# Kernel optimization log

Hardware: AMD Instinct MI355X
Metric: run time of the kernel (lower is better)

The kernel has to match this reference:

```python
import jax, jax.numpy as jnp
import numpy as np

B, S, H = 1, 2048, 4096
NQ, NKV, HD = 32, 8, 128
BLOCK = 128            # block size of block_streaming_attn_func
SINK_BLOCKS = 1        # sink_size 128 / BLOCK
LOCAL_BLOCKS = 8       # local_window_size 1024 / BLOCK
ROPE_BASE = 10000.0


def setup_inputs() -> dict:
    key = jax.random.key(0)
    ks = jax.random.split(key, 5)
    s = 0.02
    return {
        "hidden_states": jax.random.normal(ks[0], (B, S, H), jnp.float32),
        "wq": jax.random.normal(ks[1], (H, NQ * HD), jnp.float32) * s,
        "wk": jax.random.normal(ks[2], (H, NKV * HD), jnp.float32) * s,
        "wv": jax.random.normal(ks[3], (H, NKV * HD), jnp.float32) * s,
        "wo": jax.random.normal(ks[4], (NQ * HD, H), jnp.float32) * s,
    }


def _rope(x):
    # x: [B, S, heads, HD]; non-interleaved (GPT-NeoX half-split) rotary, full head_dim
    pos = jnp.arange(S, dtype=jnp.float32)
    inv = 1.0 / (ROPE_BASE ** (jnp.arange(0, HD, 2, dtype=jnp.float32) / HD))
    f = pos[:, None] * inv[None, :]                 # [S, HD/2]
    cos = jnp.cos(f)[None, :, None, :]
    sin = jnp.sin(f)[None, :, None, :]
    x1, x2 = x[..., : HD // 2], x[..., HD // 2 :]
    return jnp.concatenate([x1 * cos - x2 * sin, x2 * cos + x1 * sin], axis=-1).astype(x.dtype)


def _streaming_mask():
    # causal + (sink blocks OR local window blocks), block granularity = BLOCK
    idx = jnp.arange(S)
    blk = idx // BLOCK
    causal = idx[None, :] <= idx[:, None]
    sink = blk[None, :] < SINK_BLOCKS
    local = (blk[:, None] - blk[None, :]) < LOCAL_BLOCKS
    return causal & (sink | local)                  # [S, S]


def reference(hidden_states, wq, wk, wv, wo):
    q = (hidden_states @ wq).reshape(B, S, NQ, HD)
    k = (hidden_states @ wk).reshape(B, S, NKV, HD)
    v = (hidden_states @ wv).reshape(B, S, NKV, HD)
    q = _rope(q)
    k = _rope(k)
    rep = NQ // NKV                                 # repeat_kv (GQA)
    k = jnp.repeat(k, rep, axis=2)
    v = jnp.repeat(v, rep, axis=2)
    scores = jnp.einsum('bqhd,bkhd->bhqk', q, k) / jnp.sqrt(jnp.float32(HD))
    mask = _streaming_mask()
    scores = jnp.where(mask[None, None], scores, jnp.finfo(scores.dtype).min)
    p = jax.nn.softmax(scores, axis=-1)
    out = jnp.einsum('bhqk,bkhd->bqhd', p, v).reshape(B, S, NQ * HD)
    return out @ wo
```

## Files before the change

kernel.cpp:

```cpp
#include <hip/hip_runtime.h>
#include <hip/hip_bf16.h>
#include <math.h>

typedef __bf16 bf16;
typedef __attribute__((ext_vector_type(8))) __bf16 bf16x8;
typedef __attribute__((ext_vector_type(4))) __bf16 bf16x4;
typedef __attribute__((ext_vector_type(4))) float f32x4;

#define MFMA16(a, b, c) __builtin_amdgcn_mfma_f32_16x16x32_bf16(a, b, c, 0, 0, 0)

__device__ __forceinline__ void load16_lds(const bf16* g, bf16* l) {
  __builtin_amdgcn_global_load_lds(
      (const __attribute__((address_space(1))) void*)g,
      (__attribute__((address_space(3))) void*)l, 16, 0, 0);
}

__global__ __launch_bounds__(256) void cast_k(const float* __restrict__ src,
                                              bf16* __restrict__ dst) {
  const size_t i = ((size_t)blockIdx.x * 256 + threadIdx.x) * 8;
  f32x4 a = *(const f32x4*)(src + i);
  f32x4 b = *(const f32x4*)(src + i + 4);
  bf16x8 h;
#pragma unroll
  for (int j = 0; j < 4; ++j) {
    h[j] = (bf16)a[j];
    h[4 + j] = (bf16)b[j];
  }
  *(bf16x8*)(dst + i) = h;
}

__global__ __launch_bounds__(256) void transpose_cast_k(
    const float* __restrict__ src, bf16* __restrict__ dst, int rows,
    int cols) {
  __shared__ float tile[64][65];
  const int c0 = blockIdx.x * 64, r0 = blockIdx.y * 64;
  const int tid = threadIdx.x;
  const int lr = tid >> 4;
  const int lc = (tid & 15) * 4;
#pragma unroll
  for (int i = 0; i < 4; ++i) {
    const int row = lr + i * 16;
    const f32x4 v = *(const f32x4*)&src[(size_t)(r0 + row) * cols + c0 + lc];
#pragma unroll
    for (int j = 0; j < 4; ++j) tile[row][lc + j] = v[j];
  }
  __syncthreads();
#pragma unroll
  for (int i = 0; i < 4; ++i) {
    const int orow = lr + i * 16;
    bf16x4 h;
#pragma unroll
    for (int j = 0; j < 4; ++j) h[j] = (bf16)tile[lc + j][orow];
    *(bf16x4*)&dst[(size_t)(c0 + orow) * rows + r0 + lc] = h;
  }
}

#define BARX() __builtin_amdgcn_s_barrier()
#define LGKM0() asm volatile("s_waitcnt lgkmcnt(0)" ::: "memory")
#define VMC7() asm volatile("s_waitcnt vmcnt(7)" ::: "memory")
#define VMC6() asm volatile("s_waitcnt vmcnt(6)" ::: "memory")
#define VMC0() asm volatile("s_waitcnt vmcnt(0)" ::: "memory")

#define DS_A(BUF, QM)                                                       \
  {                                                                         \
    _Pragma("unroll") for (int mi = 0; mi < 4; ++mi)                        \
        _Pragma("unroll") for (int kk = 0; kk < 2; ++kk)                    \
            a[mi][kk] = *(const bf16x8*)&As[BUF][(aBase ^ (kk << 5)) +      \
                                                (QM)*4096 + mi * 1024];     \
  }

#define DS_B(BUF, NOFF, BR, NH)                                             \
  {                                                                         \
    _Pragma("unroll") for (int ni = 0; ni < (NH); ++ni)                     \
        _Pragma("unroll") for (int kk = 0; kk < 2; ++kk)                    \
            BR[ni][kk] = *(const bf16x8*)&Bs[BUF][(bBase ^ (kk << 5)) +     \
                                                  ((NOFF) + ni) * 1024];    \
  }

#define MMAC(QM, NOFF, BR, NH)                                              \
  {                                                                         \
    __builtin_amdgcn_s_setprio(1);                                          \
    _Pragma("unroll") for (int mi = 0; mi < 4; ++mi)                        \
        _Pragma("unroll") for (int ni = 0; ni < (NH); ++ni) {               \
      acc[(QM)*4 + mi][(NOFF) + ni] =                                       \
          MFMA16(a[mi][0], BR[ni][0], acc[(QM)*4 + mi][(NOFF) + ni]);       \
      acc[(QM)*4 + mi][(NOFF) + ni] =                                       \
          MFMA16(a[mi][1], BR[ni][1], acc[(QM)*4 + mi][(NOFF) + ni]);       \
    }                                                                       \
    __builtin_amdgcn_s_setprio(0);                                          \
  }

#define STAGE_A(BUF, T)                                                     \
  {                                                                         \
    const bf16* g0 = aS0 + (size_t)(T)*64;                                  \
    const bf16* g1 = aS1 + (size_t)(T)*64;                                  \
    bf16* l = &As[BUF][w * 512];                                            \
    load16_lds(g0, l);                                                      \
    load16_lds(g1, l + 4096);                                               \
    load16_lds(g0 + ROWK128, l + 8192);                                     \
    load16_lds(g1 + ROWK128, l + 12288);                                    \
  }

#define STAGE_B(BUF, T)                                                     \
  {                                                                         \
    _Pragma("unroll") for (int j = 0; j < NFRAG; ++j)                       \
        load16_lds(bS0 + (size_t)(T)*64 + (size_t)j * 64 * K,               \
                   &Bs[BUF][j * 4096 + w * 512]);                           \
  }

template <typename OT, int NFRAG, int EPI>
__global__ __launch_bounds__(512, 2) void gemm256(
    const bf16* __restrict__ A, const bf16* __restrict__ Bt,
    OT* __restrict__ C, bf16* __restrict__ Ck, bf16* __restrict__ Cv, int K,
    int ldc) {
  constexpr int BN = NFRAG * 64;
  constexpr int BH0 = (NFRAG + 1) / 2;
  constexpr int BH1 = NFRAG - BH0;
  const size_t ROWK128 = (size_t)128 * K;
  __shared__ bf16 As[2][256 * 64];
  __shared__ bf16 Bs[2][BN * 64];

  const int tid = threadIdx.x;
  const int lane = tid & 63;
  const int w = tid >> 6;
  const int wm = w >> 2;
  const int wn = w & 3;
  const int quad = lane >> 4;
  const int m16 = lane & 15;

  const int rowBase = blockIdx.y * 256;
  const int colBase = blockIdx.x * BN;

  const int u0 = tid, u1 = 512 + tid;
  const int r0 = u0 >> 3, c0s = (u0 & 7) ^ (r0 & 7);
  const int r1 = u1 >> 3, c1s = (u1 & 7) ^ (r1 & 7);
  const bf16* aS0 = A + (size_t)(rowBase + r0) * K + c0s * 8;
  const bf16* aS1 = A + (size_t)(rowBase + r1) * K + c1s * 8;
  const bf16* bS0 = Bt + (size_t)(colBase + r0) * K + c0s * 8;

  const int xsw = (m16 & 7) << 3;
  const int ko0 = (quad * 8) ^ xsw;
  const int aBase = (wm * 128 + m16) * 64 + ko0;
  const int bBase = (wn * (16 * NFRAG) + m16) * 64 + ko0;

  f32x4 acc[8][NFRAG];
#pragma unroll
  for (int i = 0; i < 8; ++i)
#pragma unroll
    for (int j = 0; j < NFRAG; ++j) acc[i][j] = (f32x4){0.f, 0.f, 0.f, 0.f};

  bf16x8 a[4][2], b0[BH0][2], b1[BH1 > 0 ? BH1 : 1][2];

  STAGE_A(0, 0);
  STAGE_B(0, 0);
  STAGE_A(1, 1);
  STAGE_B(1, 1);
  if constexpr (NFRAG == 3) VMC7(); else VMC6();
  BARX();

  const int nT = K / 64;
#pragma unroll 1
  for (int i = 0; i < nT / 2; ++i) {
    const int p0 = (2 * i + 2 < nT) ? 2 * i + 2 : 0;
    const int p1 = (2 * i + 3 < nT) ? 2 * i + 3 : 0;
    DS_A(0, 0);
    DS_B(0, 0, b0, BH0);
    BARX();
    LGKM0();
    MMAC(0, 0, b0, BH0);
    BARX();
    DS_B(0, BH0, b1, BH1);
    BARX();
    LGKM0();
    MMAC(0, BH0, b1, BH1);
    BARX();
    DS_A(0, 1);
    STAGE_B(0, p0);
    BARX();
    LGKM0();
    MMAC(1, 0, b0, BH0);
    BARX();
    STAGE_A(0, p0);
    if constexpr (NFRAG == 3) VMC7(); else VMC6();
    BARX();
    MMAC(1, BH0, b1, BH1);
    BARX();
    DS_A(1, 0);
    DS_B(1, 0, b0, BH0);
    BARX();
    LGKM0();
    MMAC(0, 0, b0, BH0);
    BARX();
    DS_B(1, BH0, b1, BH1);
    BARX();
    LGKM0();
    MMAC(0, BH0, b1, BH1);
    BARX();
    DS_A(1, 1);
    STAGE_B(1, p1);
    BARX();
    LGKM0();
    MMAC(1, 0, b0, BH0);
    BARX();
    STAGE_A(1, p1);
    if constexpr (NFRAG == 3) VMC7(); else VMC6();
    BARX();
    MMAC(1, BH0, b1, BH1);
    BARX();
  }
  VMC0();

#pragma unroll
  for (int am = 0; am < 8; ++am) {
    const int gr0 = rowBase + wm * 128 + am * 16 + quad * 4;
#pragma unroll
    for (int an = 0; an < NFRAG; ++an) {
      const int base16 = colBase + wn * (16 * NFRAG) + an * 16;
      const int gc = base16 + m16;
      if constexpr (EPI == 0) {
#pragma unroll
        for (int r = 0; r < 4; ++r)
          C[(size_t)(gr0 + r) * ldc + gc] = (OT)acc[am][an][r];
      } else {
        if (base16 < 4096) {
#pragma unroll
          for (int r = 0; r < 4; ++r)
            C[(size_t)(gr0 + r) * 4096 + gc] = (OT)acc[am][an][r];
        } else if (base16 < 5120) {
#pragma unroll
          for (int r = 0; r < 4; ++r)
            Ck[(size_t)(gr0 + r) * 1024 + (gc - 4096)] = (bf16)acc[am][an][r];
        } else {
          bf16x4 h;
#pragma unroll
          for (int r = 0; r < 4; ++r) h[r] = (bf16)acc[am][an][r];
          *(bf16x4*)&Cv[(size_t)(gc - 5120) * 2048 + gr0] = h;
        }
      }
    }
  }
}

__global__ __launch_bounds__(256) void rope_k(bf16* __restrict__ qb,
                                              bf16* __restrict__ kb) {
  const int NQTOT = 2048 * 32 * 64;
  const int NKTOT = 2048 * 8 * 64;
  int idx = blockIdx.x * 256 + threadIdx.x;
  bf16* buf;
  int nh, rest;
  if (idx < NQTOT) {
    buf = qb;
    nh = 32;
    rest = idx;
  } else {
    rest = idx - NQTOT;
    if (rest >= NKTOT) return;
    buf = kb;
    nh = 8;
  }
  const int j = rest & 63;
  const int hs = rest >> 6;
  const int hh = hs % nh;
  const int s = hs / nh;
  const float inv = __expf((float)j * -0.14391157f);
  const float f = (float)s * inv;
  float sn, cs;
  __sincosf(f, &sn, &cs);
  const size_t base = (size_t)(s * nh + hh) * 128 + j;
  const float x1 = (float)buf[base];
  const float x2 = (float)buf[base + 64];
  buf[base] = (bf16)(x1 * cs - x2 * sn);
  buf[base + 64] = (bf16)(x2 * cs + x1 * sn);
}

__global__ __launch_bounds__(256, 2) void attn_k(const bf16* __restrict__ q,
                                                 const bf16* __restrict__ kbuf,
                                                 const bf16* __restrict__ vT,
                                                 bf16* __restrict__ attn) {
  const int qb = 15 - blockIdx.x;
  const int h = blockIdx.y;
  const int kvh = h >> 2;
  const int tid = threadIdx.x;
  const int lane = tid & 63;
  const int w = tid >> 6;
  const int quad = lane >> 4;
  const int m16 = lane & 15;

  __shared__ bf16 Ks[4][64 * 32];
  __shared__ bf16 Vs[2][128 * 32];
  __shared__ bf16 Ps[128][72];

  const int qrow0 = qb * 128 + w * 32;

  bf16x8 qf[2][4];
#pragma unroll
  for (int rt = 0; rt < 2; ++rt)
#pragma unroll
    for (int kt = 0; kt < 4; ++kt)
      qf[rt][kt] = *(const bf16x8*)&q[(size_t)(qrow0 + rt * 16 + m16) * 4096 +
                                      h * 128 + kt * 32 + quad * 8];

  f32x4 o[2][8];
  float lsum[2][4];
#pragma unroll
  for (int rt = 0; rt < 2; ++rt) {
#pragma unroll
    for (int dt = 0; dt < 8; ++dt) o[rt][dt] = (f32x4){0.f, 0.f, 0.f, 0.f};
#pragma unroll
    for (int r = 0; r < 4; ++r) lsum[rt][r] = 0.f;
  }

  const float scale = 0.08838834764831845f;
  const bf16* kbase = kbuf + kvh * 128;
  const bf16* vbase = vT + (size_t)(kvh * 128) * 2048;

  const int klocal = (lane >> 2);
  const int kseg = (lane & 3) * 8;

  for (int b = 0; b <= qb; ++b) {
    if (b > 0 && (qb - b) >= 8) continue;
    const bool diag = (b == qb);
    for (int half = 0; half < 2; ++half) {
      const int gk0 = b * 128 + half * 64;

#pragma unroll
      for (int i = 0; i < 4; ++i) {
        const int j = w * 4 + i;
        const int kt = j >> 2, grp = (j & 3) * 16;
        load16_lds(kbase + (size_t)(gk0 + grp + klocal) * 1024 + kt * 32 + kseg,
                   &Ks[kt][grp * 32]);
      }
#pragma unroll
      for (int i = 0; i < 4; ++i) {
        const int j = w * 4 + i;
        const int kc = j >> 3, grp = (j & 7) * 16;
        load16_lds(vbase + (size_t)(grp + klocal) * 2048 + gk0 + kc * 32 + kseg,
                   &Vs[kc][grp * 32]);
      }
      __syncthreads();

      const bool skip = diag && (half * 64 > w * 32 + 31);
      if (!skip) {
        f32x4 sc[2][4];
#pragma unroll
        for (int rt = 0; rt < 2; ++rt)
#pragma unroll
          for (int ct = 0; ct < 4; ++ct)
            sc[rt][ct] = (f32x4){0.f, 0.f, 0.f, 0.f};
#pragma unroll
        for (int kt = 0; kt < 4; ++kt) {
          bf16x8 kf[4];
#pragma unroll
          for (int ct = 0; ct < 4; ++ct)
            kf[ct] = *(const bf16x8*)&Ks[kt][(ct * 16 + m16) * 32 + quad * 8];
#pragma unroll
          for (int rt = 0; rt < 2; ++rt)
#pragma unroll
            for (int ct = 0; ct < 4; ++ct)
              sc[rt][ct] = MFMA16(qf[rt][kt], kf[ct], sc[rt][ct]);
        }

#pragma unroll
        for (int rt = 0; rt < 2; ++rt)
#pragma unroll
          for (int ct = 0; ct < 4; ++ct)
#pragma unroll
            for (int r = 0; r < 4; ++r) {
              float p = __expf(sc[rt][ct][r] * scale);
              if (diag) {
                const int colg = gk0 + ct * 16 + m16;
                const int rowg = qrow0 + rt * 16 + quad * 4 + r;
                if (colg > rowg) p = 0.f;
              }
              lsum[rt][r] += p;
              Ps[w * 32 + rt * 16 + quad * 4 + r][ct * 16 + m16] = (bf16)p;
            }

#pragma unroll
        for (int rt = 0; rt < 2; ++rt)
#pragma unroll
          for (int kc = 0; kc < 2; ++kc) {
            const bf16x8 pa =
                *(const bf16x8*)&Ps[w * 32 + rt * 16 + m16][kc * 32 + quad * 8];
#pragma unroll
            for (int dt = 0; dt < 8; ++dt) {
              const bf16x8 vb =
                  *(const bf16x8*)&Vs[kc][(dt * 16 + m16) * 32 + quad * 8];
              o[rt][dt] = MFMA16(pa, vb, o[rt][dt]);
            }
          }
      }
      __syncthreads();
    }
  }

#pragma unroll
  for (int rt = 0; rt < 2; ++rt) {
    float inv[4];
#pragma unroll
    for (int r = 0; r < 4; ++r) {
      float s = lsum[rt][r];
      s += __shfl_xor(s, 1);
      s += __shfl_xor(s, 2);
      s += __shfl_xor(s, 4);
      s += __shfl_xor(s, 8);
      inv[r] = 1.0f / s;
    }
#pragma unroll
    for (int dt = 0; dt < 8; ++dt)
#pragma unroll
      for (int r = 0; r < 4; ++r)
        attn[(size_t)(qrow0 + rt * 16 + quad * 4 + r) * 4096 + h * 128 +
             dt * 16 + m16] = (bf16)(o[rt][dt][r] * inv[r]);
  }
}

extern "C" void kernel_launch(void* const* d_in, const int* in_sizes, int n_in,
                              void* d_out, int out_size, void* d_ws,
                              size_t ws_size, hipStream_t stream) {
  const float* hidden = (const float*)d_in[0];
  const float* wq = (const float*)d_in[1];
  const float* wk = (const float*)d_in[2];
  const float* wv = (const float*)d_in[3];
  const float* wo = (const float*)d_in[4];
  float* out = (float*)d_out;

  const size_t MB = 1024 * 1024;
  bf16* hiddenB = (bf16*)d_ws;
  bf16* wqkvT = (bf16*)((char*)d_ws + 16 * MB);
  bf16* woT = (bf16*)d_ws;
  bf16* attnb = (bf16*)((char*)d_ws + 32 * MB);
  bf16* qbuf = (bf16*)((char*)d_ws + 64 * MB);
  bf16* kbuf = (bf16*)((char*)d_ws + 80 * MB);
  bf16* vT = (bf16*)((char*)d_ws + 84 * MB);

  cast_k<<<4096, 256, 0, stream>>>(hidden, hiddenB);
  transpose_cast_k<<<dim3(64, 64), 256, 0, stream>>>(wq, wqkvT, 4096, 4096);
  transpose_cast_k<<<dim3(16, 64), 256, 0, stream>>>(
      wk, wqkvT + (size_t)4096 * 4096, 4096, 1024);
  transpose_cast_k<<<dim3(16, 64), 256, 0, stream>>>(
      wv, wqkvT + (size_t)5120 * 4096, 4096, 1024);

  gemm256<bf16, 3, 2><<<dim3(32, 8), 512, 0, stream>>>(hiddenB, wqkvT, qbuf,
                                                       kbuf, vT, 4096, 4096);

  rope_k<<<(2048 * 32 * 64 + 2048 * 8 * 64) / 256, 256, 0, stream>>>(qbuf,
                                                                     kbuf);

  transpose_cast_k<<<dim3(64, 64), 256, 0, stream>>>(wo, woT, 4096, 4096);

  attn_k<<<dim3(16, 32), 256, 0, stream>>>(qbuf, kbuf, vT, attnb);

  gemm256<float, 2, 0><<<dim3(32, 8), 512, 0, stream>>>(
      attnb, woT, out, nullptr, nullptr, 4096, 4096);
}
```

Before: 448.9 us.

## Restructure GEMM main loop into 4-phase schedule with staggered A/B staging

The 256-row GEMM main loop now loads all B fragments at once instead of in two halves. It also staggers the A and B tile loads into LDS so A and B are staged at different phases. Each iteration drops from 16 barrier-separated MFMA phases to 4, with tighter vmcnt waits. This aims to cut barrier and wait overhead and overlap global-to-LDS copies with MFMA work, at the cost of more live B registers and a more delicate buffer-reuse ordering.

```diff
diff --git a/kernel.cpp b/kernel.cpp
--- a/kernel.cpp
+++ b/kernel.cpp
@@ -57,9 +57,15 @@
 
 #define BARX() __builtin_amdgcn_s_barrier()
 #define LGKM0() asm volatile("s_waitcnt lgkmcnt(0)" ::: "memory")
-#define VMC7() asm volatile("s_waitcnt vmcnt(7)" ::: "memory")
-#define VMC6() asm volatile("s_waitcnt vmcnt(6)" ::: "memory")
 #define VMC0() asm volatile("s_waitcnt vmcnt(0)" ::: "memory")
+#define VMCN()                                           \
+  {                                                      \
+    if constexpr (NFRAG == 3) {                          \
+      asm volatile("s_waitcnt vmcnt(3)" ::: "memory");   \
+    } else {                                             \
+      asm volatile("s_waitcnt vmcnt(2)" ::: "memory");   \
+    }                                                    \
+  }
 
 #define DS_A(BUF, QM)                                                       \
   {                                                                         \
@@ -69,23 +75,21 @@
                                                 (QM)*4096 + mi * 1024];     \
   }
 
-#define DS_B(BUF, NOFF, BR, NH)                                             \
+#define DS_B(BUF)                                                           \
   {                                                                         \
-    _Pragma("unroll") for (int ni = 0; ni < (NH); ++ni)                     \
+    _Pragma("unroll") for (int ni = 0; ni < NFRAG; ++ni)                    \
         _Pragma("unroll") for (int kk = 0; kk < 2; ++kk)                    \
-            BR[ni][kk] = *(const bf16x8*)&Bs[BUF][(bBase ^ (kk << 5)) +     \
-                                                  ((NOFF) + ni) * 1024];    \
-  }
-
-#define MMAC(QM, NOFF, BR, NH)                                              \
+            b[ni][kk] = *(const bf16x8*)&Bs[BUF][(bBase ^ (kk << 5)) +      \
+                                                 ni * 1024];                \
+  }
+
+#define MMAC(QM)                                                            \
   {                                                                         \
     __builtin_amdgcn_s_setprio(1);                                          \
     _Pragma("unroll") for (int mi = 0; mi < 4; ++mi)                        \
-        _Pragma("unroll") for (int ni = 0; ni < (NH); ++ni) {               \
-      acc[(QM)*4 + mi][(NOFF) + ni] =                                       \
-          MFMA16(a[mi][0], BR[ni][0], acc[(QM)*4 + mi][(NOFF) + ni]);       \
-      acc[(QM)*4 + mi][(NOFF) + ni] =                                       \
-          MFMA16(a[mi][1], BR[ni][1], acc[(QM)*4 + mi][(NOFF) + ni]);       \
+        _Pragma("unroll") for (int ni = 0; ni < NFRAG; ++ni) {              \
+      acc[(QM)*4 + mi][ni] = MFMA16(a[mi][0], b[ni][0], acc[(QM)*4 + mi][ni]); \
+      acc[(QM)*4 + mi][ni] = MFMA16(a[mi][1], b[ni][1], acc[(QM)*4 + mi][ni]); \
     }                                                                       \
     __builtin_amdgcn_s_setprio(0);                                          \
   }
@@ -103,9 +107,9 @@
 
 #define STAGE_B(BUF, T)                                                     \
   {                                                                         \
-    _Pragma("unroll") for (int j = 0; j < NFRAG; ++j)                       \
-        load16_lds(bS0 + (size_t)(T)*64 + (size_t)j * 64 * K,               \
-                   &Bs[BUF][j * 4096 + w * 512]);                           \
+    _Pragma("unroll") for (int jj = 0; jj < NFRAG; ++jj)                    \
+        load16_lds(bS0 + (size_t)(T)*64 + (size_t)jj * 64 * K,              \
+                   &Bs[BUF][jj * 4096 + w * 512]);                          \
   }
 
 template <typename OT, int NFRAG, int EPI>
@@ -114,8 +118,6 @@
     OT* __restrict__ C, bf16* __restrict__ Ck, bf16* __restrict__ Cv, int K,
     int ldc) {
   constexpr int BN = NFRAG * 64;
-  constexpr int BH0 = (NFRAG + 1) / 2;
-  constexpr int BH1 = NFRAG - BH0;
   const size_t ROWK128 = (size_t)128 * K;
   __shared__ bf16 As[2][256 * 64];
   __shared__ bf16 Bs[2][BN * 64];
@@ -149,63 +151,43 @@
 #pragma unroll
     for (int j = 0; j < NFRAG; ++j) acc[i][j] = (f32x4){0.f, 0.f, 0.f, 0.f};
 
-  bf16x8 a[4][2], b0[BH0][2], b1[BH1 > 0 ? BH1 : 1][2];
-
+  bf16x8 a[4][2], b[NFRAG][2];
+
+  STAGE_B(0, 0);
   STAGE_A(0, 0);
-  STAGE_B(0, 0);
-  STAGE_A(1, 1);
   STAGE_B(1, 1);
-  if constexpr (NFRAG == 3) VMC7(); else VMC6();
+  VMCN();
   BARX();
 
   const int nT = K / 64;
 #pragma unroll 1
-  for (int i = 0; i < nT / 2; ++i) {
-    const int p0 = (2 * i + 2 < nT) ? 2 * i + 2 : 0;
-    const int p1 = (2 * i + 3 < nT) ? 2 * i + 3 : 0;
+  for (int j = 0; j < nT / 2; ++j) {
+    const int pO1 = 2 * j + 1;
+    const int pE = (2 * j + 2 < nT) ? 2 * j + 2 : 0;
+    const int pO2 = (2 * j + 3 < nT) ? 2 * j + 3 : 0;
+    DS_B(0);
     DS_A(0, 0);
-    DS_B(0, 0, b0, BH0);
-    BARX();
+    STAGE_A(1, pO1);
     LGKM0();
-    MMAC(0, 0, b0, BH0);
-    BARX();
-    DS_B(0, BH0, b1, BH1);
-    BARX();
-    LGKM0();
-    MMAC(0, BH0, b1, BH1);
+    MMAC(0);
     BARX();
     DS_A(0, 1);
-    STAGE_B(0, p0);
+    STAGE_B(0, pE);
+    VMCN();
+    LGKM0();
+    MMAC(1);
     BARX();
+    DS_B(1);
+    DS_A(1, 0);
+    STAGE_A(0, pE);
     LGKM0();
-    MMAC(1, 0, b0, BH0);
-    BARX();
-    STAGE_A(0, p0);
-    if constexpr (NFRAG == 3) VMC7(); else VMC6();
-    BARX();
-    MMAC(1, BH0, b1, BH1);
-    BARX();
-    DS_A(1, 0);
-    DS_B(1, 0, b0, BH0);
-    BARX();
-    LGKM0();
-    MMAC(0, 0, b0, BH0);
-    BARX();
-    DS_B(1, BH0, b1, BH1);
-    BARX();
-    LGKM0();
-    MMAC(0, BH0, b1, BH1);
+    MMAC(0);
     BARX();
     DS_A(1, 1);
-    STAGE_B(1, p1);
-    BARX();
+    STAGE_B(1, pO2);
+    VMCN();
     LGKM0();
-    MMAC(1, 0, b0, BH0);
-    BARX();
-    STAGE_A(1, p1);
-    if constexpr (NFRAG == 3) VMC7(); else VMC6();
-    BARX();
-    MMAC(1, BH0, b1, BH1);
+    MMAC(1);
     BARX();
   }
   VMC0();
```

After: 436.6 us. -2.7%, faster.
